# Performance work log

Hardware: AMD Instinct MI355X
Metric: run time of the kernel (lower is better)

Reference implementation:

```python
import jax, jax.numpy as jnp
import numpy as np

NUM_NODES = 50000
NUM_EDGES = 800000
HIDDEN = 128
HEADS = 8
HEAD_DIM = HIDDEN // HEADS  # 16
FF_HIDDEN = 4 * HIDDEN
LN_EPS = 1e-5


def _xavier(key, shape, gain=0.01):
    fan_out, fan_in = shape
    bound = gain * np.sqrt(6.0 / (fan_in + fan_out))
    return jax.random.uniform(key, shape, jnp.float32, -bound, bound)


def setup_inputs() -> dict:
    key = jax.random.key(0)
    ks = jax.random.split(key, 10)
    x = jax.random.normal(ks[0], (NUM_NODES, HIDDEN), jnp.float32)
    edge_index = jax.random.randint(ks[1], (2, NUM_EDGES), 0, NUM_NODES, jnp.int64)
    return {
        "x": x,
        "edge_index": edge_index,
        "Wq": _xavier(ks[2], (HIDDEN, HIDDEN)),
        "bq": jnp.zeros((HIDDEN,), jnp.float32),
        "Wk": _xavier(ks[3], (HIDDEN, HIDDEN)),
        "bk": jnp.zeros((HIDDEN,), jnp.float32),
        "Wv": _xavier(ks[4], (HIDDEN, HIDDEN)),
        "bv": jnp.zeros((HIDDEN,), jnp.float32),
        "Wo": _xavier(ks[5], (HIDDEN, HIDDEN)),
        "bo": jnp.zeros((HIDDEN,), jnp.float32),
        "W1": _xavier(ks[6], (FF_HIDDEN, HIDDEN)),
        "b1": jnp.zeros((FF_HIDDEN,), jnp.float32),
        "W2": _xavier(ks[7], (HIDDEN, FF_HIDDEN)),
        "b2": jnp.zeros((HIDDEN,), jnp.float32),
        "g1": jnp.ones((HIDDEN,), jnp.float32),
        "be1": jnp.zeros((HIDDEN,), jnp.float32),
        "g2": jnp.ones((HIDDEN,), jnp.float32),
        "be2": jnp.zeros((HIDDEN,), jnp.float32),
    }


def _layernorm(v, g, b):
    mu = jnp.mean(v, axis=-1, keepdims=True)
    var = jnp.mean(jnp.square(v - mu), axis=-1, keepdims=True)
    return (v - mu) * jax.lax.rsqrt(var + LN_EPS) * g + b


def _forward(x, edge_index, Wq, bq, Wk, bk, Wv, bv, Wo, bo, W1, b1, W2, b2, g1, be1, g2, be2):
    src = edge_index[0]  # key/value side (_j)
    dst = edge_index[1]  # query side (_i), aggregation index
    scale = 1.0 / np.sqrt(HEAD_DIM)

    # Euclidean manifold: GeometricLinear == plain linear
    q = (x @ Wq.T + bq).reshape(NUM_NODES, HEADS, HEAD_DIM)
    k = (x @ Wk.T + bk).reshape(NUM_NODES, HEADS, HEAD_DIM)
    v = (x @ Wv.T + bv).reshape(NUM_NODES, HEADS, HEAD_DIM)

    # per-edge attention scores [E, H]
    alpha = jnp.einsum('ehd,ehd->eh', q[dst], k[src]) * scale
    # segment softmax over destination nodes
    m = jax.ops.segment_max(alpha, dst, num_segments=NUM_NODES)  # [N, H]
    ea = jnp.exp(alpha - m[dst])
    denom = jax.ops.segment_sum(ea, dst, num_segments=NUM_NODES)  # [N, H]
    alpha = ea / (denom[dst] + 1e-16)

    # scatter-add weighted values -> [N, H, D]
    agg = jax.ops.segment_sum(v[src] * alpha[..., None], dst, num_segments=NUM_NODES)
    att = agg.reshape(NUM_NODES, HIDDEN) @ Wo.T + bo

    # residual + norm1 (Euclidean)
    h = _layernorm(x + att, g1, be1)

    # feed-forward: fc1 -> exact GELU -> fc2
    ff = (jax.nn.gelu(h @ W1.T + b1, approximate=False)) @ W2.T + b2

    # residual + norm2
    return _layernorm(h + ff, g2, be2)


def reference(x, edge_index, Wq, bq, Wk, bk, Wv, bv, Wo, bo, W1, b1, W2, b2, g1, be1, g2, be2):
    return _forward(x, edge_index, Wq, bq, Wk, bk, Wv, bv, Wo, bo, W1, b1, W2, b2, g1, be1, g2, be2)
```

## Files before the change

### kernel.cpp

```cpp
#include <hip/hip_runtime.h>
#include <math.h>

#define N_HEADS 8
#define HEAD_DIM 16
#define HID 128
#define QKV_ROWB 512

typedef unsigned short ushort_t;
typedef __attribute__((ext_vector_type(8))) short short8;
typedef __attribute__((ext_vector_type(4))) float floatx4;
typedef __attribute__((ext_vector_type(2))) float f32x2;

#define KV_SCALE 64.0f
#define KV_INV_SCALE 0.015625f

__device__ __forceinline__ ushort_t f2bf(float f) {
    unsigned u = __float_as_uint(f);
    unsigned r = (u + 0x7FFFu + ((u >> 16) & 1u)) >> 16;
    return (ushort_t)r;
}
__device__ __forceinline__ float bf2f(ushort_t u) {
    return __uint_as_float(((unsigned)u) << 16);
}

__device__ __forceinline__ void gld_lds16(const void* g, void* l) {
    __builtin_amdgcn_global_load_lds(
        (const __attribute__((address_space(1))) void*)g,
        (__attribute__((address_space(3))) void*)l, 16, 0, 0);
}

__device__ __forceinline__ float gelu_f(float x) {
    float z = fabsf(x) * 0.70710678118654752f;
    float t = 1.0f / (1.0f + 0.3275911f * z);
    float y = t * (0.254829592f + t * (-0.284496736f + t * (1.421413741f
            + t * (-1.453152027f + t * 1.061405429f))));
    float e = 1.0f - y * __expf(-z * z);
    e = copysignf(e, x);
    return 0.5f * x * (1.0f + e);
}

__global__ __launch_bounds__(256)
void prep_kernel(const float* __restrict__ x,
                 const float* __restrict__ Wq, const float* __restrict__ Wk,
                 const float* __restrict__ Wv, const float* __restrict__ Wo,
                 const float* __restrict__ W1, const float* __restrict__ W2,
                 const float* __restrict__ bq, const float* __restrict__ bk,
                 const float* __restrict__ bv,
                 const int* __restrict__ dst, int* __restrict__ cnt, int E,
                 ushort_t* __restrict__ xb, ushort_t* __restrict__ wts,
                 float* __restrict__ bqkv, int xpairs)
{
    int i = blockIdx.x * 256 + threadIdx.x;
    if (i < xpairs) {
        float2 v = ((const float2*)x)[i];
        xb[i * 2]     = f2bf(v.x);
        xb[i * 2 + 1] = f2bf(v.y);
        return;
    }
    int j = i - xpairs;
    if (j < 98304) {
        const float* s; int off;
        if (j < 32768) {
            if (j < 8192)       { s = Wq; off = j; }
            else if (j < 16384) { s = Wk; off = j - 8192; }
            else if (j < 24576) { s = Wv; off = j - 16384; }
            else                { s = Wo; off = j - 24576; }
        } else if (j < 65536)   { s = W1; off = j - 32768; }
        else                    { s = W2; off = j - 65536; }
        float2 v = ((const float2*)s)[off];
        wts[j * 2]     = f2bf(v.x);
        wts[j * 2 + 1] = f2bf(v.y);
        return;
    }
    int b = j - 98304;
    if (b < 384) {
        bqkv[b] = (b < 128) ? bq[b] : (b < 256) ? bk[b - 128] : bv[b - 256];
        return;
    }
    int e = b - 384;
    if (e < E) atomicAdd(&cnt[dst[e]], 1);
}

template<int MT, int ACT, int LN, int OUTF>
__global__ __launch_bounds__(256)
void gemm_t(const ushort_t* __restrict__ A, int lda, int M,
            const ushort_t* __restrict__ W, int K,
            const float* __restrict__ bias,
            float* __restrict__ outf, ushort_t* __restrict__ outb, int ostride,
            const float* __restrict__ resf, const ushort_t* __restrict__ resb,
            const float* __restrict__ g, const float* __restrict__ be)
{
    constexpr int MI  = MT / 32;
    constexpr int STG = MT * 64 + 128 * 64;
    constexpr int BNC = MT * 136;
    constexpr int SB  = STG > BNC ? STG : BNC;
    __shared__ __align__(16) ushort_t sbuf[SB];
    __shared__ float pS[LN ? MT : 1][2];
    __shared__ float pQ[LN ? MT : 1][2];
    ushort_t* As = sbuf;
    ushort_t* Ws = sbuf + MT * 64;

    const int tid  = threadIdx.x;
    const int wave = tid >> 6, lane = tid & 63;
    const int gm0 = blockIdx.x * MT;
    const int o0  = blockIdx.y * 128;
    const int mhalf = wave >> 1, ohalf = wave & 1;

    floatx4 acc[MI][4];
#pragma unroll
    for (int i = 0; i < MI; ++i)
#pragma unroll
        for (int j = 0; j < 4; ++j) acc[i][j] = (floatx4)(0.f);

    for (int kc = 0; kc < K; kc += 64) {
#pragma unroll
        for (int it = 0; it < 4; ++it) {
            int s   = it * 256 + tid;
            int ln  = s & 63;
            int grp = s >> 6;
            int tile = grp >> 1, kst = grp & 1;
            int row = tile * 16 + (ln & 15);
            int kk  = kst * 32 + (ln >> 4) * 8;
            gld_lds16(&W[(size_t)(o0 + row) * K + kc + kk],
                      &Ws[(it * 256 + wave * 64) * 8]);
        }
#pragma unroll
        for (int it = 0; it < MT / 32; ++it) {
            int s   = it * 256 + tid;
            int ln  = s & 63;
            int grp = s >> 6;
            int tile = grp >> 1, kst = grp & 1;
            int row = tile * 16 + (ln & 15);
            int kk  = kst * 32 + (ln >> 4) * 8;
            int ar = gm0 + row; if (ar >= M) ar = M - 1;
            gld_lds16(&A[(size_t)ar * lda + kc + kk],
                      &As[(it * 256 + wave * 64) * 8]);
        }
        __syncthreads();
#pragma unroll
        for (int kst = 0; kst < 2; ++kst) {
            short8 af[MI], wf[4];
#pragma unroll
            for (int i = 0; i < MI; ++i) {
                int mt = mhalf * MI + i;
                af[i] = *(const short8*)&As[((mt * 2 + kst) * 64 + lane) * 8];
            }
#pragma unroll
            for (int j = 0; j < 4; ++j) {
                int ot = ohalf * 4 + j;
                wf[j] = *(const short8*)&Ws[((ot * 2 + kst) * 64 + lane) * 8];
            }
#pragma unroll
            for (int i = 0; i < MI; ++i)
#pragma unroll
                for (int j = 0; j < 4; ++j)
                    acc[i][j] = __builtin_amdgcn_mfma_f32_16x16x32_bf16(
                        af[i], wf[j], acc[i][j], 0, 0, 0);
        }
        __syncthreads();
    }

    ushort_t* B16 = sbuf;
    float*    B32 = (float*)sbuf;

    if (LN) {
#pragma unroll
        for (int j = 0; j < 4; ++j) {
            int oc = (ohalf * 4 + j) * 16 + (lane & 15);
            float bj = bias[oc];
#pragma unroll
            for (int i = 0; i < MI; ++i) {
                int rbase = gm0 + (mhalf * MI + i) * 16 + (lane >> 4) * 4;
#pragma unroll
                for (int r = 0; r < 4; ++r) {
                    int rowc = rbase + r; if (rowc >= M) rowc = M - 1;
                    float rv = resf ? resf[(size_t)rowc * HID + oc]
                                    : bf2f(resb[(size_t)rowc * HID + oc]);
                    acc[i][j][r] += bj + rv;
                }
            }
        }
#pragma unroll
        for (int i = 0; i < MI; ++i) {
#pragma unroll
            for (int r = 0; r < 4; ++r) {
                float s1 = acc[i][0][r] + acc[i][1][r] + acc[i][2][r] + acc[i][3][r];
                float s2 = acc[i][0][r] * acc[i][0][r] + acc[i][1][r] * acc[i][1][r]
                         + acc[i][2][r] * acc[i][2][r] + acc[i][3][r] * acc[i][3][r];
                s1 += __shfl_xor(s1, 1); s1 += __shfl_xor(s1, 2);
                s1 += __shfl_xor(s1, 4); s1 += __shfl_xor(s1, 8);
                s2 += __shfl_xor(s2, 1); s2 += __shfl_xor(s2, 2);
                s2 += __shfl_xor(s2, 4); s2 += __shfl_xor(s2, 8);
                if ((lane & 15) == 0) {
                    int rl = (mhalf * MI + i) * 16 + (lane >> 4) * 4 + r;
                    pS[rl][ohalf] = s1;
                    pQ[rl][ohalf] = s2;
                }
            }
        }
        __syncthreads();
#pragma unroll
        for (int i = 0; i < MI; ++i) {
#pragma unroll
            for (int r = 0; r < 4; ++r) {
                int rl = (mhalf * MI + i) * 16 + (lane >> 4) * 4 + r;
                float S = pS[rl][0] + pS[rl][1];
                float Q = pQ[rl][0] + pQ[rl][1];
                float mu = S * (1.f / 128.f);
                float var = Q * (1.f / 128.f) - mu * mu;
                float rstd = rsqrtf(var + 1e-5f);
#pragma unroll
                for (int j = 0; j < 4; ++j) {
                    int oc = (ohalf * 4 + j) * 16 + (lane & 15);
                    acc[i][j][r] = (acc[i][j][r] - mu) * rstd * g[oc] + be[oc];
                }
            }
        }
        __syncthreads();
    }

    if (OUTF == 0) {
#pragma unroll
        for (int i = 0; i < MI; ++i)
#pragma unroll
            for (int j = 0; j < 4; ++j) {
                int oc = (ohalf * 4 + j) * 16 + (lane & 15);
                float bj = LN ? 0.f : bias[oc];
#pragma unroll
                for (int r = 0; r < 4; ++r) {
                    int rl = (mhalf * MI + i) * 16 + (lane >> 4) * 4 + r;
                    float v = acc[i][j][r] + bj;
                    if (ACT) v = gelu_f(v);
                    B16[rl * 136 + oc] = f2bf(v);
                }
            }
        __syncthreads();
#pragma unroll
        for (int p = 0; p < MT / 16; ++p) {
            int row = p * 16 + (tid >> 4);
            int ch  = tid & 15;
            if (gm0 + row < M)
                *(short8*)&outb[(size_t)(gm0 + row) * ostride + o0 + ch * 8] =
                    *(const short8*)&B16[row * 136 + ch * 8];
        }
    } else if (OUTF == 2) {
#pragma unroll
        for (int i = 0; i < MI; ++i)
#pragma unroll
            for (int j = 0; j < 4; ++j) {
                int oc = (ohalf * 4 + j) * 16 + (lane & 15);
                float bj = bias[o0 + oc];
#pragma unroll
                for (int r = 0; r < 4; ++r) {
                    int rl = (mhalf * MI + i) * 16 + (lane >> 4) * 4 + r;
                    float v = (acc[i][j][r] + bj) * KV_SCALE;
                    B16[rl * 136 + oc] = f2bf(v);
                }
            }
        __syncthreads();
        const int koff = blockIdx.y * 8;
#pragma unroll
        for (int p = 0; p < MT / 16; ++p) {
            int row = p * 16 + (tid >> 4);
            int ch  = tid & 15;
            if (gm0 + row < M) {
                short8 s = *(const short8*)&B16[row * 136 + ch * 8];
                unsigned u0 = 0, u1 = 0;
                u0 = __builtin_amdgcn_cvt_pk_fp8_f32(
                         bf2f((ushort_t)s[0]), bf2f((ushort_t)s[1]), u0, false);
                u0 = __builtin_amdgcn_cvt_pk_fp8_f32(
                         bf2f((ushort_t)s[2]), bf2f((ushort_t)s[3]), u0, true);
                u1 = __builtin_amdgcn_cvt_pk_fp8_f32(
                         bf2f((ushort_t)s[4]), bf2f((ushort_t)s[5]), u1, false);
                u1 = __builtin_amdgcn_cvt_pk_fp8_f32(
                         bf2f((ushort_t)s[6]), bf2f((ushort_t)s[7]), u1, true);
                uint2 o; o.x = u0; o.y = u1;
                *(uint2*)((char*)outb + (size_t)(gm0 + row) * QKV_ROWB
                          + 256 + ch * 16 + koff) = o;
            }
        }
    } else {
#pragma unroll
        for (int p = 0; p < 2; ++p) {
            if (ohalf == p) {
#pragma unroll
                for (int i = 0; i < MI; ++i)
#pragma unroll
                    for (int j = 0; j < 4; ++j) {
                        int ocl = j * 16 + (lane & 15);
                        float bj = LN ? 0.f : bias[p * 64 + ocl];
#pragma unroll
                        for (int r = 0; r < 4; ++r) {
                            int rl = (mhalf * MI + i) * 16 + (lane >> 4) * 4 + r;
                            float v = acc[i][j][r] + bj;
                            if (ACT) v = gelu_f(v);
                            B32[rl * 68 + ocl] = v;
                        }
                    }
            }
            __syncthreads();
#pragma unroll
            for (int q = 0; q < MT / 16; ++q) {
                int row = q * 16 + (tid >> 4);
                int ch  = tid & 15;
                if (gm0 + row < M)
                    *(float4*)&outf[(size_t)(gm0 + row) * ostride + o0 + p * 64 + ch * 4] =
                        *(const float4*)&B32[row * 68 + ch * 4];
            }
            __syncthreads();
        }
    }
}

__global__ __launch_bounds__(256)
void scan1_kernel(const int* __restrict__ cnt, int* __restrict__ parts, int N)
{
    __shared__ int sd[256];
    int t = threadIdx.x;
    int base = blockIdx.x * 1024 + t * 4;
    int s = 0;
#pragma unroll
    for (int j = 0; j < 4; ++j) if (base + j < N) s += cnt[base + j];
    sd[t] = s; __syncthreads();
    for (int off = 128; off; off >>= 1) {
        if (t < off) sd[t] += sd[t + off];
        __syncthreads();
    }
    if (t == 0) parts[blockIdx.x] = sd[0];
}

__global__ __launch_bounds__(256)
void scan2_kernel(const int* __restrict__ parts, int* __restrict__ poff, int nb)
{
    __shared__ int sd[256];
    int t = threadIdx.x;
    int v = (t < nb) ? parts[t] : 0;
    sd[t] = v; __syncthreads();
    for (int off = 1; off < 256; off <<= 1) {
        int u = (t >= off) ? sd[t - off] : 0;
        __syncthreads();
        sd[t] += u;
        __syncthreads();
    }
    if (t < nb) poff[t] = sd[t] - v;
}

__global__ __launch_bounds__(256)
void scan3_kernel(const int* __restrict__ cnt, const int* __restrict__ poff,
                  int* __restrict__ rp, int N)
{
    __shared__ int sd[256];
    int t = threadIdx.x;
    int base = blockIdx.x * 1024 + t * 4;
    int v0 = (base + 0 < N) ? cnt[base + 0] : 0;
    int v1 = (base + 1 < N) ? cnt[base + 1] : 0;
    int v2 = (base + 2 < N) ? cnt[base + 2] : 0;
    int v3 = (base + 3 < N) ? cnt[base + 3] : 0;
    int s = v0 + v1 + v2 + v3;
    sd[t] = s; __syncthreads();
    for (int off = 1; off < 256; off <<= 1) {
        int u = (t >= off) ? sd[t - off] : 0;
        __syncthreads();
        sd[t] += u;
        __syncthreads();
    }
    int o = poff[blockIdx.x] + sd[t] - s;
    if (base + 0 < N) rp[base + 0] = o;
    if (base + 1 < N) rp[base + 1] = o + v0;
    if (base + 2 < N) rp[base + 2] = o + v0 + v1;
    if (base + 3 < N) rp[base + 3] = o + v0 + v1 + v2;
}

__global__ __launch_bounds__(256)
void scatter_kernel(const int* __restrict__ src, const int* __restrict__ dst,
                    int* __restrict__ rp, int* __restrict__ ssrc, int E)
{
    int e = blockIdx.x * 256 + threadIdx.x;
    if (e >= E) return;
    int pos = atomicAdd(&rp[dst[e]], 1);
    ssrc[pos] = src[e];
}

__global__ __launch_bounds__(256)
void attn_fused_kernel(const ushort_t* __restrict__ qkvb, const int* __restrict__ rp,
                       const int* __restrict__ ssrc, ushort_t* __restrict__ aggb, int N)
{
    int wave = threadIdx.x >> 6, lane = threadIdx.x & 63;
    int n = blockIdx.x * 4 + wave;
    if (n >= N) return;
    int grp = lane >> 4;
    int cb  = (lane & 15) * 16;
    const char* base = (const char*)qkvb;

    short8 qv = *(const short8*)(base + n * QKV_ROWB + cb);
    float q[8];
#pragma unroll
    for (int j = 0; j < 8; ++j) q[j] = bf2f((ushort_t)qv[j]) * (0.25f / KV_SCALE);

    int r0 = n ? rp[n - 1] : 0;
    int r1 = rp[n];
    float acc[8] = {0.f, 0.f, 0.f, 0.f, 0.f, 0.f, 0.f, 0.f};
    float l = 0.f;

    int r = r0;
    for (; r + 8 <= r1; r += 8) {
        int s0 = ssrc[r + grp];
        int s1 = ssrc[r + 4 + grp];
        uint4 kv0 = *(const uint4*)(base + s0 * QKV_ROWB + 256 + cb);
        uint4 kv1 = *(const uint4*)(base + s1 * QKV_ROWB + 256 + cb);

        f32x2 a0 = __builtin_amdgcn_cvt_pk_f32_fp8(kv0.x, false);
        f32x2 a1 = __builtin_amdgcn_cvt_pk_f32_fp8(kv0.x, true);
        f32x2 a2 = __builtin_amdgcn_cvt_pk_f32_fp8(kv0.y, false);
        f32x2 a3 = __builtin_amdgcn_cvt_pk_f32_fp8(kv0.y, true);
        f32x2 b0 = __builtin_amdgcn_cvt_pk_f32_fp8(kv1.x, false);
        f32x2 b1 = __builtin_amdgcn_cvt_pk_f32_fp8(kv1.x, true);
        f32x2 b2 = __builtin_amdgcn_cvt_pk_f32_fp8(kv1.y, false);
        f32x2 b3 = __builtin_amdgcn_cvt_pk_f32_fp8(kv1.y, true);

        float p0 = 0.f, p1 = 0.f;
        p0 = fmaf(q[0], a0.x, p0); p0 = fmaf(q[1], a0.y, p0);
        p0 = fmaf(q[2], a1.x, p0); p0 = fmaf(q[3], a1.y, p0);
        p0 = fmaf(q[4], a2.x, p0); p0 = fmaf(q[5], a2.y, p0);
        p0 = fmaf(q[6], a3.x, p0); p0 = fmaf(q[7], a3.y, p0);
        p1 = fmaf(q[0], b0.x, p1); p1 = fmaf(q[1], b0.y, p1);
        p1 = fmaf(q[2], b1.x, p1); p1 = fmaf(q[3], b1.y, p1);
        p1 = fmaf(q[4], b2.x, p1); p1 = fmaf(q[5], b2.y, p1);
        p1 = fmaf(q[6], b3.x, p1); p1 = fmaf(q[7], b3.y, p1);

        p0 += __shfl_xor(p0, 1);
        p1 += __shfl_xor(p1, 1);
        float e0 = __expf(p0), e1 = __expf(p1);
        l += e0 + e1;

        f32x2 v0 = __builtin_amdgcn_cvt_pk_f32_fp8(kv0.z, false);
        f32x2 v1 = __builtin_amdgcn_cvt_pk_f32_fp8(kv0.z, true);
        f32x2 v2 = __builtin_amdgcn_cvt_pk_f32_fp8(kv0.w, false);
        f32x2 v3 = __builtin_amdgcn_cvt_pk_f32_fp8(kv0.w, true);
        f32x2 w0 = __builtin_amdgcn_cvt_pk_f32_fp8(kv1.z, false);
        f32x2 w1 = __builtin_amdgcn_cvt_pk_f32_fp8(kv1.z, true);
        f32x2 w2 = __builtin_amdgcn_cvt_pk_f32_fp8(kv1.w, false);
        f32x2 w3 = __builtin_amdgcn_cvt_pk_f32_fp8(kv1.w, true);

        acc[0] = fmaf(e0, v0.x, acc[0]); acc[1] = fmaf(e0, v0.y, acc[1]);
        acc[2] = fmaf(e0, v1.x, acc[2]); acc[3] = fmaf(e0, v1.y, acc[3]);
        acc[4] = fmaf(e0, v2.x, acc[4]); acc[5] = fmaf(e0, v2.y, acc[5]);
        acc[6] = fmaf(e0, v3.x, acc[6]); acc[7] = fmaf(e0, v3.y, acc[7]);
        acc[0] = fmaf(e1, w0.x, acc[0]); acc[1] = fmaf(e1, w0.y, acc[1]);
        acc[2] = fmaf(e1, w1.x, acc[2]); acc[3] = fmaf(e1, w1.y, acc[3]);
        acc[4] = fmaf(e1, w2.x, acc[4]); acc[5] = fmaf(e1, w2.y, acc[5]);
        acc[6] = fmaf(e1, w3.x, acc[6]); acc[7] = fmaf(e1, w3.y, acc[7]);
    }
    for (; r < r1; r += 4) {
        int e = r + grp;
        int s = ssrc[(e < r1) ? e : r0];
        uint4 kv = *(const uint4*)(base + s * QKV_ROWB + 256 + cb);
        f32x2 a0 = __builtin_amdgcn_cvt_pk_f32_fp8(kv.x, false);
        f32x2 a1 = __builtin_amdgcn_cvt_pk_f32_fp8(kv.x, true);
        f32x2 a2 = __builtin_amdgcn_cvt_pk_f32_fp8(kv.y, false);
        f32x2 a3 = __builtin_amdgcn_cvt_pk_f32_fp8(kv.y, true);
        float p = 0.f;
        p = fmaf(q[0], a0.x, p); p = fmaf(q[1], a0.y, p);
        p = fmaf(q[2], a1.x, p); p = fmaf(q[3], a1.y, p);
        p = fmaf(q[4], a2.x, p); p = fmaf(q[5], a2.y, p);
        p = fmaf(q[6], a3.x, p); p = fmaf(q[7], a3.y, p);
        p += __shfl_xor(p, 1);
        float ea = (e < r1) ? __expf(p) : 0.f;
        l += ea;
        f32x2 v0 = __builtin_amdgcn_cvt_pk_f32_fp8(kv.z, false);
        f32x2 v1 = __builtin_amdgcn_cvt_pk_f32_fp8(kv.z, true);
        f32x2 v2 = __builtin_amdgcn_cvt_pk_f32_fp8(kv.w, false);
        f32x2 v3 = __builtin_amdgcn_cvt_pk_f32_fp8(kv.w, true);
        acc[0] = fmaf(ea, v0.x, acc[0]); acc[1] = fmaf(ea, v0.y, acc[1]);
        acc[2] = fmaf(ea, v1.x, acc[2]); acc[3] = fmaf(ea, v1.y, acc[3]);
        acc[4] = fmaf(ea, v2.x, acc[4]); acc[5] = fmaf(ea, v2.y, acc[5]);
        acc[6] = fmaf(ea, v3.x, acc[6]); acc[7] = fmaf(ea, v3.y, acc[7]);
    }

#pragma unroll
    for (int j = 0; j < 8; ++j) {
        acc[j] += __shfl_xor(acc[j], 16);
        acc[j] += __shfl_xor(acc[j], 32);
    }
    l += __shfl_xor(l, 16);
    l += __shfl_xor(l, 32);
    float inv = KV_INV_SCALE / (l + 1e-16f);
    if (grp == 0) {
        short8 o;
#pragma unroll
        for (int j = 0; j < 8; ++j) o[j] = (short)f2bf(acc[j] * inv);
        *(short8*)((char*)aggb + n * 256 + cb) = o;
    }
}

extern "C" void kernel_launch(void* const* d_in, const int* in_sizes, int n_in,
                              void* d_out, int out_size, void* d_ws, size_t ws_size,
                              hipStream_t stream)
{
    const float* x  = (const float*)d_in[0];
    const int*   ei = (const int*)d_in[1];
    const float* Wq = (const float*)d_in[2];
    const float* bq = (const float*)d_in[3];
    const float* Wk = (const float*)d_in[4];
    const float* bk = (const float*)d_in[5];
    const float* Wv = (const float*)d_in[6];
    const float* bv = (const float*)d_in[7];
    const float* Wo = (const float*)d_in[8];
    const float* bo = (const float*)d_in[9];
    const float* W1 = (const float*)d_in[10];
    const float* b1 = (const float*)d_in[11];
    const float* W2 = (const float*)d_in[12];
    const float* b2 = (const float*)d_in[13];
    const float* g1 = (const float*)d_in[14];
    const float* be1= (const float*)d_in[15];
    const float* g2 = (const float*)d_in[16];
    const float* be2= (const float*)d_in[17];
    float* out = (float*)d_out;

    const int N = in_sizes[0] / HID;
    const int E = in_sizes[1] / 2;
    const int* srcp = ei;
    const int* dstp = ei + E;

    const size_t NH = (size_t)N * HID;
    float* wsf = (float*)d_ws;

    ushort_t* xb   = (ushort_t*)wsf;
    ushort_t* qkvb = (ushort_t*)(wsf + NH / 2);
    ushort_t* aggb = (ushort_t*)(wsf + 2 * NH);
    ushort_t* hb   = (ushort_t*)wsf;
    ushort_t* ffb  = (ushort_t*)(wsf + NH / 2);

    ushort_t* wts  = (ushort_t*)(wsf + 2 * NH + NH / 2);
    float*    bqkv = (float*)(wts + 196608);
    int*      rp   = (int*)(bqkv + 384);
    int*      cnt  = rp + (N + 1);
    int*      poff = cnt + N;
    int*      parts= poff + 256;
    int*      ssrc = parts + 256;

    hipMemsetAsync(cnt, 0, N * sizeof(int), stream);
    const int xpairs = (int)(NH / 2);
    const int ptot   = xpairs + 98304 + 384 + E;
    prep_kernel<<<(ptot + 255) / 256, 256, 0, stream>>>(
        x, Wq, Wk, Wv, Wo, W1, W2, bq, bk, bv, dstp, cnt, E,
        xb, wts, bqkv, xpairs);

    const int nb = (N + 1023) / 1024;
    scan1_kernel<<<nb, 256, 0, stream>>>(cnt, parts, N);
    scan2_kernel<<<1, 256, 0, stream>>>(parts, poff, nb);
    scan3_kernel<<<nb, 256, 0, stream>>>(cnt, poff, rp, N);
    scatter_kernel<<<(E + 255) / 256, 256, 0, stream>>>(srcp, dstp, rp, ssrc, E);

    const int gx64 = (N + 63) / 64;

    gemm_t<64, 0, 0, 0><<<dim3(gx64, 1), 256, 0, stream>>>(
        xb, HID, N, wts, HID, bqkv, nullptr, qkvb, 256,
        nullptr, nullptr, nullptr, nullptr);

    gemm_t<64, 0, 0, 2><<<dim3(gx64, 2), 256, 0, stream>>>(
        xb, HID, N, wts + 16384, HID, bqkv + 128, nullptr, qkvb, 0,
        nullptr, nullptr, nullptr, nullptr);

    attn_fused_kernel<<<(N + 3) / 4, 256, 0, stream>>>(qkvb, rp, ssrc, aggb, N);

    gemm_t<64, 0, 1, 0><<<dim3(gx64, 1), 256, 0, stream>>>(
        aggb, HID, N, wts + 49152, HID, bo, nullptr, hb, HID,
        x, nullptr, g1, be1);

    gemm_t<64, 1, 0, 0><<<dim3(gx64, 4), 256, 0, stream>>>(
        hb, HID, N, wts + 65536, HID, b1, nullptr, ffb, 512,
        nullptr, nullptr, nullptr, nullptr);

    gemm_t<64, 0, 1, 1><<<dim3(gx64, 1), 256, 0, stream>>>(
        ffb, 512, N, wts + 131072, 512, b2, out, nullptr, HID,
        nullptr, hb, g2, be2);
}
```

Before: 358.8 us.

## Fuse feed-forward GEMMs with LayerNorm, merge QKV GEMMs, partition scatter by destination

Adds a fused FFN kernel that keeps the 64x512 GELU intermediate in shared memory in 128-column chunks, then applies fc2, the residual and LayerNorm. This removes the global round trip of the bf16 FF activation. The Q and K/V projection GEMMs are merged into one launch using a new output mode keyed on blockIdx.y. The CSR scatter now runs as a fixed-size grid where each block group handles one eighth of the destination range, meant to localize atomics, at the cost of every group re-reading all edges. The fused FFN kernel has lower parallelism per block and redoes no work but serializes the weight loads.

```diff
diff --git a/kernel.cpp b/kernel.cpp
--- a/kernel.cpp
+++ b/kernel.cpp
@@ -219,13 +219,13 @@
         __syncthreads();
     }
 
-    if (OUTF == 0) {
+    if (OUTF == 0 || (OUTF == 3 && blockIdx.y == 0)) {
 #pragma unroll
         for (int i = 0; i < MI; ++i)
 #pragma unroll
             for (int j = 0; j < 4; ++j) {
                 int oc = (ohalf * 4 + j) * 16 + (lane & 15);
-                float bj = LN ? 0.f : bias[oc];
+                float bj = LN ? 0.f : bias[o0 + oc];
 #pragma unroll
                 for (int r = 0; r < 4; ++r) {
                     int rl = (mhalf * MI + i) * 16 + (lane >> 4) * 4 + r;
@@ -235,15 +235,16 @@
                 }
             }
         __syncthreads();
+        const int oo = (OUTF == 3) ? 0 : o0;
 #pragma unroll
         for (int p = 0; p < MT / 16; ++p) {
             int row = p * 16 + (tid >> 4);
             int ch  = tid & 15;
             if (gm0 + row < M)
-                *(short8*)&outb[(size_t)(gm0 + row) * ostride + o0 + ch * 8] =
+                *(short8*)&outb[(size_t)(gm0 + row) * ostride + oo + ch * 8] =
                     *(const short8*)&B16[row * 136 + ch * 8];
         }
-    } else if (OUTF == 2) {
+    } else if (OUTF == 2 || OUTF == 3) {
 #pragma unroll
         for (int i = 0; i < MI; ++i)
 #pragma unroll
@@ -258,7 +259,7 @@
                 }
             }
         __syncthreads();
-        const int koff = blockIdx.y * 8;
+        const int koff = (OUTF == 3) ? (blockIdx.y - 1) * 8 : blockIdx.y * 8;
 #pragma unroll
         for (int p = 0; p < MT / 16; ++p) {
             int row = p * 16 + (tid >> 4);
@@ -313,6 +314,223 @@
 }
 
 __global__ __launch_bounds__(256)
+void ff_fused_kernel(const ushort_t* __restrict__ hb,
+                     const ushort_t* __restrict__ w1,
+                     const float* __restrict__ b1,
+                     const ushort_t* __restrict__ w2,
+                     const float* __restrict__ b2,
+                     const float* __restrict__ g, const float* __restrict__ be,
+                     float* __restrict__ out, int M)
+{
+    __shared__ __align__(16) ushort_t Hs[8192];
+    __shared__ __align__(16) ushort_t Wst[8192];
+    __shared__ __align__(16) ushort_t a1t[8704];
+    __shared__ float pS[64][2];
+    __shared__ float pQ[64][2];
+
+    const int tid = threadIdx.x;
+    const int wave = tid >> 6, lane = tid & 63;
+    const int gm0 = blockIdx.x * 64;
+    const int mhalf = wave >> 1, ohalf = wave & 1;
+
+#pragma unroll
+    for (int it = 0; it < 4; ++it) {
+        int s = it * 256 + tid;
+        int l = s & 63;
+        int g8 = (s >> 6) & 7;
+        int kc = s >> 9;
+        int tile = g8 >> 1, kst = g8 & 1;
+        int row = tile * 16 + (l & 15);
+        int kk = kc * 64 + kst * 32 + (l >> 4) * 8;
+        int ar = gm0 + row; if (ar >= M) ar = M - 1;
+        gld_lds16(&hb[(size_t)ar * HID + kk], &Hs[(it * 256 + wave * 64) * 8]);
+    }
+
+    floatx4 acc2[2][4];
+#pragma unroll
+    for (int i = 0; i < 2; ++i)
+#pragma unroll
+        for (int j = 0; j < 4; ++j) acc2[i][j] = (floatx4)(0.f);
+
+    for (int c = 0; c < 4; ++c) {
+        floatx4 acc1[2][4];
+#pragma unroll
+        for (int i = 0; i < 2; ++i)
+#pragma unroll
+            for (int j = 0; j < 4; ++j) acc1[i][j] = (floatx4)(0.f);
+
+#pragma unroll
+        for (int kc = 0; kc < 2; ++kc) {
+#pragma unroll
+            for (int it = 0; it < 4; ++it) {
+                int s = it * 256 + tid;
+                int l = s & 63;
+                int grp = s >> 6;
+                int tile = grp >> 1, kst = grp & 1;
+                int row = c * 128 + tile * 16 + (l & 15);
+                int kk = kc * 64 + kst * 32 + (l >> 4) * 8;
+                gld_lds16(&w1[(size_t)row * HID + kk],
+                          &Wst[(it * 256 + wave * 64) * 8]);
+            }
+            __syncthreads();
+#pragma unroll
+            for (int kst = 0; kst < 2; ++kst) {
+                short8 af[2], wf[4];
+#pragma unroll
+                for (int i = 0; i < 2; ++i) {
+                    int mt = mhalf * 2 + i;
+                    af[i] = *(const short8*)&Hs[(((kc << 3) + mt * 2 + kst) * 64 + lane) * 8];
+                }
+#pragma unroll
+                for (int j = 0; j < 4; ++j) {
+                    int ot = ohalf * 4 + j;
+                    wf[j] = *(const short8*)&Wst[((ot * 2 + kst) * 64 + lane) * 8];
+                }
+#pragma unroll
+                for (int i = 0; i < 2; ++i)
+#pragma unroll
+                    for (int j = 0; j < 4; ++j)
+                        acc1[i][j] = __builtin_amdgcn_mfma_f32_16x16x32_bf16(
+                            af[i], wf[j], acc1[i][j], 0, 0, 0);
+            }
+            __syncthreads();
+        }
+
+#pragma unroll
+        for (int i = 0; i < 2; ++i)
+#pragma unroll
+            for (int j = 0; j < 4; ++j) {
+                int oc = (ohalf * 4 + j) * 16 + (lane & 15);
+                float bj = b1[c * 128 + oc];
+#pragma unroll
+                for (int r = 0; r < 4; ++r) {
+                    int rl = (mhalf * 2 + i) * 16 + (lane >> 4) * 4 + r;
+                    a1t[rl * 136 + oc] = f2bf(gelu_f(acc1[i][j][r] + bj));
+                }
+            }
+
+#pragma unroll
+        for (int kc2 = 0; kc2 < 2; ++kc2) {
+#pragma unroll
+            for (int it = 0; it < 4; ++it) {
+                int s = it * 256 + tid;
+                int l = s & 63;
+                int grp = s >> 6;
+                int tile = grp >> 1, kst = grp & 1;
+                int row = tile * 16 + (l & 15);
+                int kk = c * 128 + kc2 * 64 + kst * 32 + (l >> 4) * 8;
+                gld_lds16(&w2[(size_t)row * 512 + kk],
+                          &Wst[(it * 256 + wave * 64) * 8]);
+            }
+            __syncthreads();
+#pragma unroll
+            for (int kst = 0; kst < 2; ++kst) {
+                short8 af[2], wf[4];
+#pragma unroll
+                for (int i = 0; i < 2; ++i) {
+                    int mt = mhalf * 2 + i;
+                    af[i] = *(const short8*)&a1t[(mt * 16 + (lane & 15)) * 136
+                                                 + kc2 * 64 + kst * 32 + (lane >> 4) * 8];
+                }
+#pragma unroll
+                for (int j = 0; j < 4; ++j) {
+                    int ot = ohalf * 4 + j;
+                    wf[j] = *(const short8*)&Wst[((ot * 2 + kst) * 64 + lane) * 8];
+                }
+#pragma unroll
+                for (int i = 0; i < 2; ++i)
+#pragma unroll
+                    for (int j = 0; j < 4; ++j)
+                        acc2[i][j] = __builtin_amdgcn_mfma_f32_16x16x32_bf16(
+                            af[i], wf[j], acc2[i][j], 0, 0, 0);
+            }
+            __syncthreads();
+        }
+    }
+
+#pragma unroll
+    for (int j = 0; j < 4; ++j) {
+        int oc = (ohalf * 4 + j) * 16 + (lane & 15);
+        float bj = b2[oc];
+#pragma unroll
+        for (int i = 0; i < 2; ++i) {
+#pragma unroll
+            for (int r = 0; r < 4; ++r) {
+                int rl = (mhalf * 2 + i) * 16 + (lane >> 4) * 4 + r;
+                float rv = bf2f(Hs[(((oc >> 6) * 8 + (rl >> 4) * 2 + ((oc >> 5) & 1)) * 64
+                                    + (rl & 15) + ((oc >> 3) & 3) * 16) * 8 + (oc & 7)]);
+                acc2[i][j][r] += bj + rv;
+            }
+        }
+    }
+#pragma unroll
+    for (int i = 0; i < 2; ++i) {
+#pragma unroll
+        for (int r = 0; r < 4; ++r) {
+            float s1 = acc2[i][0][r] + acc2[i][1][r] + acc2[i][2][r] + acc2[i][3][r];
+            float s2 = acc2[i][0][r] * acc2[i][0][r] + acc2[i][1][r] * acc2[i][1][r]
+                     + acc2[i][2][r] * acc2[i][2][r] + acc2[i][3][r] * acc2[i][3][r];
+            s1 += __shfl_xor(s1, 1); s1 += __shfl_xor(s1, 2);
+            s1 += __shfl_xor(s1, 4); s1 += __shfl_xor(s1, 8);
+            s2 += __shfl_xor(s2, 1); s2 += __shfl_xor(s2, 2);
+            s2 += __shfl_xor(s2, 4); s2 += __shfl_xor(s2, 8);
+            if ((lane & 15) == 0) {
+                int rl = (mhalf * 2 + i) * 16 + (lane >> 4) * 4 + r;
+                pS[rl][ohalf] = s1;
+                pQ[rl][ohalf] = s2;
+            }
+        }
+    }
+    __syncthreads();
+#pragma unroll
+    for (int i = 0; i < 2; ++i) {
+#pragma unroll
+        for (int r = 0; r < 4; ++r) {
+            int rl = (mhalf * 2 + i) * 16 + (lane >> 4) * 4 + r;
+            float S = pS[rl][0] + pS[rl][1];
+            float Q = pQ[rl][0] + pQ[rl][1];
+            float mu = S * (1.f / 128.f);
+            float var = Q * (1.f / 128.f) - mu * mu;
+            float rstd = rsqrtf(var + 1e-5f);
+#pragma unroll
+            for (int j = 0; j < 4; ++j) {
+                int oc = (ohalf * 4 + j) * 16 + (lane & 15);
+                acc2[i][j][r] = (acc2[i][j][r] - mu) * rstd * g[oc] + be[oc];
+            }
+        }
+    }
+    __syncthreads();
+
+    float* B32 = (float*)a1t;
+#pragma unroll
+    for (int p = 0; p < 2; ++p) {
+        if (ohalf == p) {
+#pragma unroll
+            for (int i = 0; i < 2; ++i)
+#pragma unroll
+                for (int j = 0; j < 4; ++j) {
+                    int ocl = j * 16 + (lane & 15);
+#pragma unroll
+                    for (int r = 0; r < 4; ++r) {
+                        int rl = (mhalf * 2 + i) * 16 + (lane >> 4) * 4 + r;
+                        B32[rl * 68 + ocl] = acc2[i][j][r];
+                    }
+                }
+        }
+        __syncthreads();
+#pragma unroll
+        for (int q = 0; q < 4; ++q) {
+            int row = q * 16 + (tid >> 4);
+            int ch  = tid & 15;
+            if (gm0 + row < M)
+                *(float4*)&out[(size_t)(gm0 + row) * HID + p * 64 + ch * 4] =
+                    *(const float4*)&B32[row * 68 + ch * 4];
+        }
+        __syncthreads();
+    }
+}
+
+__global__ __launch_bounds__(256)
 void scan1_kernel(const int* __restrict__ cnt, int* __restrict__ parts, int N)
 {
     __shared__ int sd[256];
@@ -373,12 +591,21 @@
 
 __global__ __launch_bounds__(256)
 void scatter_kernel(const int* __restrict__ src, const int* __restrict__ dst,
-                    int* __restrict__ rp, int* __restrict__ ssrc, int E)
-{
-    int e = blockIdx.x * 256 + threadIdx.x;
-    if (e >= E) return;
-    int pos = atomicAdd(&rp[dst[e]], 1);
-    ssrc[pos] = src[e];
+                    int* __restrict__ rp, int* __restrict__ ssrc, int E, int N)
+{
+    int coh = blockIdx.x & 7;
+    int bc  = blockIdx.x >> 3;
+    int rr  = (N + 7) >> 3;
+    int nlo = coh * rr;
+    int nhi = nlo + rr; if (nhi > N) nhi = N;
+    int stride = (gridDim.x >> 3) * 256;
+    for (int e = bc * 256 + threadIdx.x; e < E; e += stride) {
+        int d = dst[e];
+        if (d >= nlo && d < nhi) {
+            int pos = atomicAdd(&rp[d], 1);
+            ssrc[pos] = src[e];
+        }
+    }
 }
 
 __global__ __launch_bounds__(256)
@@ -529,7 +756,6 @@
     ushort_t* qkvb = (ushort_t*)(wsf + NH / 2);
     ushort_t* aggb = (ushort_t*)(wsf + 2 * NH);
     ushort_t* hb   = (ushort_t*)wsf;
-    ushort_t* ffb  = (ushort_t*)(wsf + NH / 2);
 
     ushort_t* wts  = (ushort_t*)(wsf + 2 * NH + NH / 2);
     float*    bqkv = (float*)(wts + 196608);
@@ -550,16 +776,12 @@
     scan1_kernel<<<nb, 256, 0, stream>>>(cnt, parts, N);
     scan2_kernel<<<1, 256, 0, stream>>>(parts, poff, nb);
     scan3_kernel<<<nb, 256, 0, stream>>>(cnt, poff, rp, N);
-    scatter_kernel<<<(E + 255) / 256, 256, 0, stream>>>(srcp, dstp, rp, ssrc, E);
+    scatter_kernel<<<2048, 256, 0, stream>>>(srcp, dstp, rp, ssrc, E, N);
 
     const int gx64 = (N + 63) / 64;
 
-    gemm_t<64, 0, 0, 0><<<dim3(gx64, 1), 256, 0, stream>>>(
+    gemm_t<64, 0, 0, 3><<<dim3(gx64, 3), 256, 0, stream>>>(
         xb, HID, N, wts, HID, bqkv, nullptr, qkvb, 256,
-        nullptr, nullptr, nullptr, nullptr);
-
-    gemm_t<64, 0, 0, 2><<<dim3(gx64, 2), 256, 0, stream>>>(
-        xb, HID, N, wts + 16384, HID, bqkv + 128, nullptr, qkvb, 0,
         nullptr, nullptr, nullptr, nullptr);
 
     attn_fused_kernel<<<(N + 3) / 4, 256, 0, stream>>>(qkvb, rp, ssrc, aggb, N);
@@ -568,11 +790,6 @@
         aggb, HID, N, wts + 49152, HID, bo, nullptr, hb, HID,
         x, nullptr, g1, be1);
 
-    gemm_t<64, 1, 0, 0><<<dim3(gx64, 4), 256, 0, stream>>>(
-        hb, HID, N, wts + 65536, HID, b1, nullptr, ffb, 512,
-        nullptr, nullptr, nullptr, nullptr);
-
-    gemm_t<64, 0, 1, 1><<<dim3(gx64, 1), 256, 0, stream>>>(
-        ffb, 512, N, wts + 131072, 512, b2, out, nullptr, HID,
-        nullptr, hb, g2, be2);
-}
+    ff_fused_kernel<<<gx64, 256, 0, stream>>>(
+        hb, wts + 65536, b1, wts + 131072, b2, g2, be2, out, N);
+}
```

Result: faster. 336.9 us (-6.1%).
